# Optimization experiments

Hardware: AMD Instinct MI355X
Metric: run time of the kernel (lower is better)

The kernel has to match this reference:

```python
import jax, jax.numpy as jnp
import numpy as np

WIN = 9  # local window size per spatial dim

def _boxfilter3d(x):
    k = jnp.ones((1, 1, WIN, WIN, WIN), x.dtype) / float(WIN ** 3)
    return jax.lax.conv_general_dilated(
        x, k, window_strides=(1, 1, 1), padding='SAME',
        dimension_numbers=('NCDHW', 'OIDHW', 'NCDHW'))

def setup_inputs() -> dict:
    key = jax.random.key(0)
    k1, k2 = jax.random.split(key)
    shape = (2, 1, 160, 192, 160)
    y_true = jax.random.uniform(k1, shape, dtype=jnp.float32)
    y_pred = jax.random.uniform(k2, shape, dtype=jnp.float32)
    return {"y_true": y_true, "y_pred": y_pred}

def reference(y_true, y_pred):
    Ii, Ji = y_true, y_pred
    mu1 = _boxfilter3d(Ii)
    mu2 = _boxfilter3d(Ji)
    sigma1_sq = _boxfilter3d(Ii * Ii) - mu1 * mu1
    sigma2_sq = _boxfilter3d(Ji * Ji) - mu2 * mu2
    sigma12 = _boxfilter3d(Ii * Ji) - mu1 * mu2
    cc = (sigma12 * sigma12) / (sigma1_sq * sigma2_sq + 1e-5)
    return -jnp.mean(cc)
```

## Files before the change

kernel.cpp:

```cpp
#include <hip/hip_runtime.h>

#define DD 160
#define HH 192
#define WW 160
#define HWs (HH * WW)
#define NTOT 9830400.0f
#define DOUT 40
#define NIT  48
#define NBLK 480

typedef float    v4 __attribute__((ext_vector_type(4)));
typedef float    v8 __attribute__((ext_vector_type(8)));
typedef _Float16 h4 __attribute__((ext_vector_type(4)));
typedef _Float16 h8 __attribute__((ext_vector_type(8)));

__global__ __launch_bounds__(256, 2) void kf(const float* __restrict__ I,
                                             const float* __restrict__ J,
                                             float* __restrict__ partial) {
    __shared__ float rawb[2][2][24][40];
    __shared__ h4    hsb[2][5][16][10];
    __shared__ h8    ring[9][5][64];

    const int tid = threadIdx.x;
    const int bx  = blockIdx.x;
    const int b   = blockIdx.z;
    const int tx  = bx % 5, ty = bx / 5;
    const int w0 = tx * 32, h0 = ty * 16;
    const int d0 = blockIdx.y * DOUT;
    const int bid = bx + 60 * (blockIdx.y + 4 * b);

    const int  rtid = tid ^ ((bx & 1) << 7);
    const bool isW  = (rtid >= 192);
    const bool isH  = (rtid < 160);
    const int  p    = rtid & 63;
    const int  wr   = p >> 2, wg8 = p & 3;
    const int  hr   = rtid / 10, hk = rtid % 10;

    const int  uA   = tid;
    const int  qA   = (uA < 240) ? uA : uA - 240;
    const int  inpA = (uA < 240) ? 0 : 1;
    const int  rowA = qA / 10, gA = qA % 10;
    const int  ghA = h0 - 4 + rowA, gwA = w0 - 4 + gA * 4;
    const bool okA = (ghA >= 0 && ghA < HH && gwA >= 0 && gwA < WW);
    const size_t offA = (size_t)ghA * WW + gwA;
    const int  ldsA = inpA * 960 + rowA * 40 + gA * 4;
    const float* srcA = inpA ? J : I;

    const bool hasB = (tid < 224);
    const int  qB   = tid + 16;
    const int  rowB = qB / 10, gB = qB % 10;
    const int  ghB = h0 - 4 + rowB, gwB = w0 - 4 + gB * 4;
    const bool okB = hasB && (ghB >= 0 && ghB < HH && gwB >= 0 && gwB < WW);
    const size_t offB = (size_t)ghB * WW + gwB;
    const int  ldsB = 960 + rowB * 40 + gB * 4;

    float* rawF = &rawb[0][0][0][0];
    const size_t base_b = (size_t)b * DD * HWs;

    v4 pA = (v4)0.f, pB = (v4)0.f;
    {
        const int s0 = d0 - 4;
        if (s0 >= 0) {
            const size_t sb = base_b + (size_t)s0 * HWs;
            if (okA) pA = *(const v4*)(srcA + sb + offA);
            if (okB) pB = *(const v4*)(J + sb + offB);
        }
    }

    v8 S[5] = {(v8)0.f, (v8)0.f, (v8)0.f, (v8)0.f, (v8)0.f};
    v8 accv = (v8)0.f;
    int wslot = 0;
    const float inv = 1.0f / 729.0f;

    for (int t = 0; t <= NIT; ++t) {
        const int  si  = d0 - 4 + t;
        const bool sv  = (t < NIT) && (si >= 0 && si < DD);
        const int  par = t & 1;

        if (sv) {
            *(v4*)(rawF + par * 1920 + ldsA) = pA;
            if (hasB) *(v4*)(rawF + par * 1920 + ldsB) = pB;
        }
        if (t + 1 < NIT) {
            const int sn = si + 1;
            if (sn >= 0 && sn < DD) {
                const size_t sb = base_b + (size_t)sn * HWs;
                pA = okA ? *(const v4*)(srcA + sb + offA) : (v4)0.f;
                if (hasB) pB = okB ? *(const v4*)(J + sb + offB) : (v4)0.f;
            }
        }
        __syncthreads();

        if (sv && isH) {
            v4 sI = (v4)0.f, sJ = (v4)0.f, sII = (v4)0.f, sJJ = (v4)0.f,
               sIJ = (v4)0.f;
#pragma unroll
            for (int tt = 0; tt < 9; ++tt) {
                v4 a  = *(const v4*)&rawb[par][0][hr + tt][hk * 4];
                v4 bb = *(const v4*)&rawb[par][1][hr + tt][hk * 4];
                sI += a; sJ += bb; sII += a * a; sJJ += bb * bb; sIJ += a * bb;
            }
            hsb[par][0][hr][hk] = __builtin_convertvector(sI,  h4);
            hsb[par][1][hr][hk] = __builtin_convertvector(sJ,  h4);
            hsb[par][2][hr][hk] = __builtin_convertvector(sII, h4);
            hsb[par][3][hr][hk] = __builtin_convertvector(sJJ, h4);
            hsb[par][4][hr][hk] = __builtin_convertvector(sIJ, h4);
        }

        if (t >= 1 && isW) {
            const int tp  = t - 1;
            const int sip = d0 - 4 + tp;
            v8 o[5];
            if (sip >= 0 && sip < DD) {
                const int pb = tp & 1;
#pragma unroll
                for (int c = 0; c < 5; ++c) {
                    const h4* hp = &hsb[pb][c][wr][wg8 * 2];
                    v8 fa = __builtin_convertvector(*(const h8*)hp, v8);
                    v8 fb = __builtin_convertvector(*(const h8*)(hp + 2), v8);
                    float s = fa[0] + fa[1] + fa[2] + fa[3] + fa[4] + fa[5] +
                              fa[6] + fa[7] + fb[0];
                    v8 ov; ov[0] = s;
                    s = s - fa[0] + fb[1]; ov[1] = s;
                    s = s - fa[1] + fb[2]; ov[2] = s;
                    s = s - fa[2] + fb[3]; ov[3] = s;
                    s = s - fa[3] + fb[4]; ov[4] = s;
                    s = s - fa[4] + fb[5]; ov[5] = s;
                    s = s - fa[5] + fb[6]; ov[6] = s;
                    s = s - fa[6] + fb[7]; ov[7] = s;
                    o[c] = ov;
                }
            } else {
#pragma unroll
                for (int c = 0; c < 5; ++c) o[c] = (v8)0.f;
            }
#pragma unroll
            for (int c = 0; c < 5; ++c) {
                h8 nv = __builtin_convertvector(o[c], h8);
                if (tp >= 9)
                    S[c] -= __builtin_convertvector(ring[wslot][c][p], v8);
                ring[wslot][c][p] = nv;
                S[c] += __builtin_convertvector(nv, v8);
            }
            if (++wslot == 9) wslot = 0;

            if (tp >= 8) {
                v8 mu1 = S[0] * inv, mu2 = S[1] * inv;
                v8 g1  = S[2] * inv - mu1 * mu1;
                v8 g2  = S[3] * inv - mu2 * mu2;
                v8 g12 = S[4] * inv - mu1 * mu2;
                v8 num = g12 * g12;
                v8 den = g1 * g2 + 1e-5f;
#pragma unroll
                for (int e = 0; e < 8; ++e)
                    accv[e] += __fdividef(num[e], den[e]);
            }
        }
    }

    if (isW) {
        float a = accv[0] + accv[1] + accv[2] + accv[3] +
                  accv[4] + accv[5] + accv[6] + accv[7];
#pragma unroll
        for (int off = 32; off > 0; off >>= 1) a += __shfl_down(a, off);
        if (p == 0) partial[bid] = a;
    }
}

__global__ void k3_final(const float* __restrict__ partial,
                         float* __restrict__ out) {
    __shared__ float r[512];
    const int i = threadIdx.x;
    r[i] = (i < NBLK) ? partial[i] : 0.f;
    __syncthreads();
    for (int off = 256; off > 0; off >>= 1) {
        if (i < off) r[i] += r[i + off];
        __syncthreads();
    }
    if (i == 0) out[0] = -r[0] * (1.0f / NTOT);
}

extern "C" void kernel_launch(void* const* d_in, const int* in_sizes, int n_in,
                              void* d_out, int out_size, void* d_ws, size_t ws_size,
                              hipStream_t stream) {
    (void)in_sizes; (void)n_in; (void)out_size; (void)ws_size;
    const float* I = (const float*)d_in[0];
    const float* J = (const float*)d_in[1];
    float* out     = (float*)d_out;
    float* partial = (float*)d_ws;

    dim3 grid(60, 4, 2);
    kf<<<grid, 256, 0, stream>>>(I, J, partial);
    k3_final<<<1, 512, 0, stream>>>(partial, out);
}
```

Baseline: 163.5 us.

## Deepen global prefetch to two slices and sync only on LDS counters

Register prefetch of input slices goes from one slice ahead to two, so each global load has about two iterations to complete. The __syncthreads is replaced by a custom barrier that waits only on LDS/scalar counters (vmcnt left unwaited), so in-flight global loads no longer stall the barrier. This costs extra registers under a 256x2 launch bound. It also depends on the compiler placing correct vmcnt waits before the prefetched registers are used.

```diff
diff --git a/kernel.cpp b/kernel.cpp
--- a/kernel.cpp
+++ b/kernel.cpp
@@ -13,6 +13,11 @@
 typedef float    v8 __attribute__((ext_vector_type(8)));
 typedef _Float16 h4 __attribute__((ext_vector_type(4)));
 typedef _Float16 h8 __attribute__((ext_vector_type(8)));
+
+__device__ __forceinline__ void block_sync_lds() {
+    __builtin_amdgcn_s_waitcnt(0xc07f);
+    __builtin_amdgcn_s_barrier();
+}
 
 __global__ __launch_bounds__(256, 2) void kf(const float* __restrict__ I,
                                              const float* __restrict__ J,
@@ -57,13 +62,19 @@
     float* rawF = &rawb[0][0][0][0];
     const size_t base_b = (size_t)b * DD * HWs;
 
-    v4 pA = (v4)0.f, pB = (v4)0.f;
+    v4 p0A = (v4)0.f, p0B = (v4)0.f, p1A = (v4)0.f, p1B = (v4)0.f;
     {
         const int s0 = d0 - 4;
         if (s0 >= 0) {
             const size_t sb = base_b + (size_t)s0 * HWs;
-            if (okA) pA = *(const v4*)(srcA + sb + offA);
-            if (okB) pB = *(const v4*)(J + sb + offB);
+            if (okA) p0A = *(const v4*)(srcA + sb + offA);
+            if (okB) p0B = *(const v4*)(J + sb + offB);
+        }
+        const int s1 = d0 - 3;
+        if (s1 >= 0) {
+            const size_t sb = base_b + (size_t)s1 * HWs;
+            if (okA) p1A = *(const v4*)(srcA + sb + offA);
+            if (okB) p1B = *(const v4*)(J + sb + offB);
         }
     }
 
@@ -78,18 +89,19 @@
         const int  par = t & 1;
 
         if (sv) {
-            *(v4*)(rawF + par * 1920 + ldsA) = pA;
-            if (hasB) *(v4*)(rawF + par * 1920 + ldsB) = pB;
-        }
-        if (t + 1 < NIT) {
-            const int sn = si + 1;
-            if (sn >= 0 && sn < DD) {
+            *(v4*)(rawF + par * 1920 + ldsA) = p0A;
+            if (hasB) *(v4*)(rawF + par * 1920 + ldsB) = p0B;
+        }
+        p0A = p1A; p0B = p1B;
+        {
+            const int sn = si + 2;
+            if (t + 2 < NIT && sn >= 0 && sn < DD) {
                 const size_t sb = base_b + (size_t)sn * HWs;
-                pA = okA ? *(const v4*)(srcA + sb + offA) : (v4)0.f;
-                if (hasB) pB = okB ? *(const v4*)(J + sb + offB) : (v4)0.f;
-            }
-        }
-        __syncthreads();
+                p1A = okA ? *(const v4*)(srcA + sb + offA) : (v4)0.f;
+                if (hasB) p1B = okB ? *(const v4*)(J + sb + offB) : (v4)0.f;
+            }
+        }
+        block_sync_lds();
 
         if (sv && isH) {
             v4 sI = (v4)0.f, sJ = (v4)0.f, sII = (v4)0.f, sJJ = (v4)0.f,
```

New measurement: 167.3 us. +2.3%, slower.
